# Kernel optimization log

Measured on AMD Instinct MI355X. Metric: run time of the kernel, lower is better.

Reference implementation:

```python
import jax, jax.numpy as jnp
import numpy as np

B, D, L, H = 256, 512, 64, 300


def setup_inputs() -> dict:
    key = jax.random.key(0)
    ks = jax.random.split(key, 16)
    s = 0.05  # weight init scale to keep activations sane through ReLU chains
    return {
        "x": jax.random.normal(ks[0], (B, D), jnp.float32),
        "eps": jax.random.normal(ks[1], (B, L), jnp.float32),
        "W": jax.random.normal(ks[2], (D, L), jnp.float32) * s,
        "enc1_w": jax.random.normal(ks[3], (H, D), jnp.float32) * s,
        "enc1_b": jax.random.normal(ks[4], (H,), jnp.float32) * s,
        "enc2_w": jax.random.normal(ks[5], (H, H), jnp.float32) * s,
        "enc2_b": jax.random.normal(ks[6], (H,), jnp.float32) * s,
        "zm_w": jax.random.normal(ks[7], (L, H), jnp.float32) * s,
        "zm_b": jax.random.normal(ks[8], (L,), jnp.float32) * s,
        "zv_w": jax.random.normal(ks[9], (L, H), jnp.float32) * s,
        "zv_b": jax.random.normal(ks[10], (L,), jnp.float32) * s,
        "gen1_w": jax.random.normal(ks[11], (H, L), jnp.float32) * s,
        "gen2_w": jax.random.normal(ks[12], (H, H), jnp.float32) * s,
        "gen2_b": jax.random.normal(ks[13], (H,), jnp.float32) * s,
        "head_w": jax.random.normal(ks[14], (D, H), jnp.float32) * s,
        "head_b": jax.random.normal(ks[15], (D,), jnp.float32) * s,
    }


def reference(x, eps, W, enc1_w, enc1_b, enc2_w, enc2_b, zm_w, zm_b,
              zv_w, zv_b, gen1_w, gen2_w, gen2_b, head_w, head_b):
    # encode: q_z = ReLU(Linear) -> ReLU(Linear)
    h = jax.nn.relu(x @ enc1_w.T + enc1_b)
    h = jax.nn.relu(h @ enc2_w.T + enc2_b)
    z_mean = h @ zm_w.T + zm_b          # [B, L]
    z_log_var = h @ zv_w.T + zv_b       # [B, L]
    # reparameterize (eps passed in for determinism)
    z = z_mean + eps * jnp.exp(0.5 * z_log_var)
    # decode: per-column masked z through shared generator + per-column head,
    # vectorized over the column axis D (mask = W rows)
    masked = z[:, None, :] * W[None, :, :]                       # [B, D, L]
    g1 = jax.nn.relu(jnp.einsum('bdl,hl->bdh', masked, gen1_w))  # [B, D, H]
    g2 = jax.nn.relu(jnp.einsum('bdh,gh->bdg', g1, gen2_w) + gen2_b)
    x_mean = jnp.einsum('bdh,dh->bd', g2, head_w) + head_b       # [B, D]
    return (x_mean, z, z_mean, z_log_var)
```

## Files before the change

### kernel.cpp

```cpp
#include <hip/hip_runtime.h>

typedef unsigned short u16;
typedef unsigned int u32;

typedef __bf16 bf16x8 __attribute__((ext_vector_type(8)));
typedef float f32x4 __attribute__((ext_vector_type(4)));

union V16 { uint4 u; bf16x8 v; u16 s[8]; };
union F4  { float4 v; float f[4]; };

__device__ __forceinline__ float bf2f(u16 a) {
  union { u32 u; float f; } c; c.u = ((u32)a) << 16; return c.f;
}
__device__ __forceinline__ u16 f2bf(float f) {
  union { float f; u32 u; } c; c.f = f;
  u32 u = c.u;
  u += 0x7fffu + ((u >> 16) & 1u);
  return (u16)(u >> 16);
}

#define Z_OFF   131072
#define ZM_OFF  147456
#define ZLV_OFF 163840

#define B1_OFF 0
#define B2_OFF 2560
#define E1_OFF 15360
#define E2_OFF 35840
#define ZMP_OFF 48640
#define ZVP_OFF 51200
#define PACK_TOTAL 53760

__device__ __forceinline__ void pack_one(const float* __restrict__ src,
                                         int t, int s, int lane,
                                         int Nsrc, int Ksrc, int rowlen,
                                         uint4* __restrict__ dst) {
  const int n = t * 16 + (lane & 15);
  const int k0 = s * 32 + ((lane >> 4) << 3);
  V16 v;
#pragma unroll
  for (int j = 0; j < 8; ++j) {
    const int k = k0 + j;
    v.s[j] = (n < Nsrc && k < Ksrc) ? f2bf(src[n * rowlen + k]) : (u16)0;
  }
  *dst = v.u;
}

__global__ __launch_bounds__(256) void pack_kernel(
    const float* __restrict__ g1w, const float* __restrict__ g2w,
    const float* __restrict__ e1w, const float* __restrict__ e2w,
    const float* __restrict__ zmw, const float* __restrict__ zvw,
    uint4* __restrict__ ws4) {
  const int idx = blockIdx.x * 256 + threadIdx.x;
  if (idx >= PACK_TOTAL) return;
  const int lane = idx & 63;
  if (idx < B2_OFF) {
    const int f = (idx - B1_OFF) >> 6;
    pack_one(g1w, f >> 1, f & 1, lane, 300, 64, 64, ws4 + idx);
  } else if (idx < E1_OFF) {
    const int f = (idx - B2_OFF) >> 6;
    pack_one(g2w, f / 10, f % 10, lane, 300, 300, 300, ws4 + idx);
  } else if (idx < E2_OFF) {
    const int f = (idx - E1_OFF) >> 6;
    pack_one(e1w, f >> 4, f & 15, lane, 300, 512, 512, ws4 + idx);
  } else if (idx < ZMP_OFF) {
    const int f = (idx - E2_OFF) >> 6;
    pack_one(e2w, f / 10, f % 10, lane, 300, 300, 300, ws4 + idx);
  } else if (idx < ZVP_OFF) {
    const int f = (idx - ZMP_OFF) >> 6;
    pack_one(zmw, f / 10, f % 10, lane, 64, 300, 300, ws4 + idx);
  } else {
    const int f = (idx - ZVP_OFF) >> 6;
    pack_one(zvw, f / 10, f % 10, lane, 64, 300, 300, ws4 + idx);
  }
}

__global__ __launch_bounds__(640, 3) void enc_kernel(
    const float* __restrict__ x, const float* __restrict__ eps,
    const uint4* __restrict__ e1p, const float* __restrict__ e1b,
    const uint4* __restrict__ e2p, const float* __restrict__ e2b,
    const uint4* __restrict__ zmp, const float* __restrict__ zmb,
    const uint4* __restrict__ zvp, const float* __restrict__ zvb,
    float* __restrict__ out) {
  __shared__ u16 h1s[16 * 328];
  __shared__ u16 h2s[16 * 328];
  __shared__ float zms[1024], zlvs[1024];
  const int bi0 = blockIdx.x * 16;
  const int tid = threadIdx.x;
  const int w = tid >> 6, lane = tid & 63, q = lane >> 4, c = lane & 15;

  bf16x8 af[16];
#pragma unroll
  for (int s = 0; s < 16; ++s) {
    const float* px = x + (bi0 + c) * 512 + s * 32 + q * 8;
    F4 a, b; a.v = *(const float4*)px; b.v = *(const float4*)(px + 4);
    V16 m;
#pragma unroll
    for (int j = 0; j < 4; ++j) { m.s[j] = f2bf(a.f[j]); m.s[4 + j] = f2bf(b.f[j]); }
    af[s] = m.v;
  }
  f32x4 acc0 = {0.f, 0.f, 0.f, 0.f}, acc1 = {0.f, 0.f, 0.f, 0.f};
  for (int s = 0; s < 16; ++s) {
    V16 b0, b1;
    b0.u = e1p[((2 * w + 0) * 16 + s) * 64 + lane];
    b1.u = e1p[((2 * w + 1) * 16 + s) * 64 + lane];
    acc0 = __builtin_amdgcn_mfma_f32_16x16x32_bf16(af[s], b0.v, acc0, 0, 0, 0);
    acc1 = __builtin_amdgcn_mfma_f32_16x16x32_bf16(af[s], b1.v, acc1, 0, 0, 0);
  }
#pragma unroll
  for (int tt = 0; tt < 2; ++tt) {
    const f32x4 acc = tt ? acc1 : acc0;
    const int col = (2 * w + tt) * 16 + c;
    const float bias = (col < 300) ? e1b[col] : 0.f;
#pragma unroll
    for (int i = 0; i < 4; ++i)
      h1s[(4 * q + i) * 328 + col] = (col < 300) ? f2bf(fmaxf(acc[i] + bias, 0.f)) : (u16)0;
  }
  __syncthreads();
  acc0 = {0.f, 0.f, 0.f, 0.f}; acc1 = {0.f, 0.f, 0.f, 0.f};
  for (int s = 0; s < 10; ++s) {
    V16 a; a.u = *(const uint4*)&h1s[c * 328 + s * 32 + q * 8];
    V16 b0, b1;
    b0.u = e2p[((2 * w + 0) * 10 + s) * 64 + lane];
    b1.u = e2p[((2 * w + 1) * 10 + s) * 64 + lane];
    acc0 = __builtin_amdgcn_mfma_f32_16x16x32_bf16(a.v, b0.v, acc0, 0, 0, 0);
    acc1 = __builtin_amdgcn_mfma_f32_16x16x32_bf16(a.v, b1.v, acc1, 0, 0, 0);
  }
#pragma unroll
  for (int tt = 0; tt < 2; ++tt) {
    const f32x4 acc = tt ? acc1 : acc0;
    const int col = (2 * w + tt) * 16 + c;
    const float bias = (col < 300) ? e2b[col] : 0.f;
#pragma unroll
    for (int i = 0; i < 4; ++i)
      h2s[(4 * q + i) * 328 + col] = (col < 300) ? f2bf(fmaxf(acc[i] + bias, 0.f)) : (u16)0;
  }
  __syncthreads();
  if (w < 8) {
    const bool is_m = (w < 4);
    const int t = w & 3;
    const uint4* hp = is_m ? zmp : zvp;
    f32x4 a4 = {0.f, 0.f, 0.f, 0.f};
    for (int s = 0; s < 10; ++s) {
      V16 a; a.u = *(const uint4*)&h2s[c * 328 + s * 32 + q * 8];
      V16 b; b.u = hp[(t * 10 + s) * 64 + lane];
      a4 = __builtin_amdgcn_mfma_f32_16x16x32_bf16(a.v, b.v, a4, 0, 0, 0);
    }
    const int col = t * 16 + c;
    const float bias = is_m ? zmb[col] : zvb[col];
    float* dst = is_m ? zms : zlvs;
#pragma unroll
    for (int i = 0; i < 4; ++i) dst[(4 * q + i) * 64 + col] = a4[i] + bias;
  }
  __syncthreads();
  for (int idx = tid; idx < 1024; idx += 640) {
    const int row = idx >> 6, col = idx & 63;
    const int gi = (bi0 + row) * 64 + col;
    const float zm = zms[idx], zlv = zlvs[idx];
    const float zz = zm + eps[gi] * expf(0.5f * zlv);
    out[Z_OFF + gi] = zz;
    out[ZM_OFF + gi] = zm;
    out[ZLV_OFF + gi] = zlv;
  }
}

__global__ __launch_bounds__(640, 3) void dec_kernel(
    const float* __restrict__ z,
    const float* __restrict__ W,
    const uint4* __restrict__ b1p,
    const uint4* __restrict__ b2p,
    const float* __restrict__ g2b,
    const float* __restrict__ hw,
    const float* __restrict__ hb,
    float* __restrict__ xout)
{
  __shared__ u16 g1s[128 * 328];
  __shared__ float xred[5][128];

  const int wg = blockIdx.x;
  const int r0 = wg << 7;
  const int bi = r0 >> 9;
  const int d0 = r0 & 511;
  const int tid = threadIdx.x;
  const int w = tid >> 6;
  const int lane = tid & 63;
  const int q = lane >> 4;
  const int c = lane & 15;
  const int u = w >> 1;
  const int v = w & 1;

  const float* zrow = z + bi * 64;

  bf16x8 bz[4][2];
#pragma unroll
  for (int kf = 0; kf < 2; ++kf) {
    F4 z0, z1;
    z0.v = *(const float4*)(zrow + kf * 32 + q * 8);
    z1.v = *(const float4*)(zrow + kf * 32 + q * 8 + 4);
#pragma unroll
    for (int tt = 0; tt < 4; ++tt) {
      V16 r; r.u = b1p[((4 * u + tt) * 2 + kf) * 64 + lane];
      V16 m;
#pragma unroll
      for (int j = 0; j < 4; ++j) {
        m.s[j]     = f2bf(bf2f(r.s[j])     * z0.f[j]);
        m.s[4 + j] = f2bf(bf2f(r.s[4 + j]) * z1.f[j]);
      }
      bz[tt][kf] = m.v;
    }
  }
  for (int rt = 0; rt < 4; ++rt) {
    const int rowA = v * 64 + rt * 16 + c;
    const float* p = W + (d0 + rowA) * 64 + q * 8;
    bf16x8 af0, af1;
    {
      F4 a, b; V16 m;
      a.v = *(const float4*)p; b.v = *(const float4*)(p + 4);
#pragma unroll
      for (int j = 0; j < 4; ++j) { m.s[j] = f2bf(a.f[j]); m.s[4 + j] = f2bf(b.f[j]); }
      af0 = m.v;
      a.v = *(const float4*)(p + 32); b.v = *(const float4*)(p + 36);
#pragma unroll
      for (int j = 0; j < 4; ++j) { m.s[j] = f2bf(a.f[j]); m.s[4 + j] = f2bf(b.f[j]); }
      af1 = m.v;
    }
    f32x4 acc[4];
#pragma unroll
    for (int tt = 0; tt < 4; ++tt) acc[tt] = {0.f, 0.f, 0.f, 0.f};
#pragma unroll
    for (int tt = 0; tt < 4; ++tt) {
      acc[tt] = __builtin_amdgcn_mfma_f32_16x16x32_bf16(af0, bz[tt][0], acc[tt], 0, 0, 0);
      acc[tt] = __builtin_amdgcn_mfma_f32_16x16x32_bf16(af1, bz[tt][1], acc[tt], 0, 0, 0);
    }
    const int rwb = v * 64 + rt * 16 + 4 * q;
#pragma unroll
    for (int tt = 0; tt < 4; ++tt) {
      const int colb = (4 * u + tt) * 16 + c;
#pragma unroll
      for (int i = 0; i < 4; ++i)
        g1s[(rwb + i) * 328 + colb] = f2bf(fmaxf(acc[tt][i], 0.f));
    }
  }
  __syncthreads();

  f32x4 a3[4][4];
#pragma unroll
  for (int tt = 0; tt < 4; ++tt)
#pragma unroll
    for (int rt = 0; rt < 4; ++rt) a3[tt][rt] = {0.f, 0.f, 0.f, 0.f};
  for (int s = 0; s < 10; ++s) {
    V16 b[4];
#pragma unroll
    for (int tt = 0; tt < 4; ++tt) b[tt].u = b2p[((4 * u + tt) * 10 + s) * 64 + lane];
#pragma unroll
    for (int rt = 0; rt < 4; ++rt) {
      V16 a; a.u = *(const uint4*)&g1s[(v * 64 + rt * 16 + c) * 328 + s * 32 + q * 8];
#pragma unroll
      for (int tt = 0; tt < 4; ++tt)
        a3[tt][rt] = __builtin_amdgcn_mfma_f32_16x16x32_bf16(a.v, b[tt].v, a3[tt][rt], 0, 0, 0);
    }
  }
  float xacc[4][4];
#pragma unroll
  for (int rt = 0; rt < 4; ++rt)
#pragma unroll
    for (int i = 0; i < 4; ++i) xacc[rt][i] = 0.f;
#pragma unroll
  for (int tt = 0; tt < 4; ++tt) {
    const int col = (4 * u + tt) * 16 + c;
    const bool inb = (col < 300);
    const float bias = inb ? g2b[col] : 0.f;
#pragma unroll
    for (int rt = 0; rt < 4; ++rt)
#pragma unroll
      for (int i = 0; i < 4; ++i) {
        const float g2v = fmaxf(a3[tt][rt][i] + bias, 0.f);
        const float h = inb ? hw[(d0 + v * 64 + rt * 16 + 4 * q + i) * 300 + col] : 0.f;
        xacc[rt][i] += g2v * h;
      }
  }
#pragma unroll
  for (int rt = 0; rt < 4; ++rt)
#pragma unroll
    for (int i = 0; i < 4; ++i) {
      float t = xacc[rt][i];
      t += __shfl_xor(t, 1);
      t += __shfl_xor(t, 2);
      t += __shfl_xor(t, 4);
      t += __shfl_xor(t, 8);
      xacc[rt][i] = t;
    }
  if (c < 4) {
#pragma unroll
    for (int rt = 0; rt < 4; ++rt) {
      float t = xacc[rt][0];
      t = (c == 1) ? xacc[rt][1] : t;
      t = (c == 2) ? xacc[rt][2] : t;
      t = (c == 3) ? xacc[rt][3] : t;
      xred[u][v * 64 + rt * 16 + 4 * q + c] = t;
    }
  }
  __syncthreads();
  if (tid < 128) {
    float t = hb[d0 + tid];
#pragma unroll
    for (int uu = 0; uu < 5; ++uu) t += xred[uu][tid];
    xout[r0 + tid] = t;
  }
}

extern "C" void kernel_launch(void* const* d_in, const int* in_sizes, int n_in,
                              void* d_out, int out_size, void* d_ws, size_t ws_size,
                              hipStream_t stream) {
  const float* x   = (const float*)d_in[0];
  const float* eps = (const float*)d_in[1];
  const float* W   = (const float*)d_in[2];
  const float* e1w = (const float*)d_in[3];
  const float* e1b = (const float*)d_in[4];
  const float* e2w = (const float*)d_in[5];
  const float* e2b = (const float*)d_in[6];
  const float* zmw = (const float*)d_in[7];
  const float* zmb = (const float*)d_in[8];
  const float* zvw = (const float*)d_in[9];
  const float* zvb = (const float*)d_in[10];
  const float* g1w = (const float*)d_in[11];
  const float* g2w = (const float*)d_in[12];
  const float* g2b = (const float*)d_in[13];
  const float* hw  = (const float*)d_in[14];
  const float* hb  = (const float*)d_in[15];
  float* out = (float*)d_out;
  uint4* ws4 = (uint4*)d_ws;

  pack_kernel<<<(PACK_TOTAL + 255) / 256, 256, 0, stream>>>(g1w, g2w, e1w, e2w, zmw, zvw, ws4);
  enc_kernel<<<16, 640, 0, stream>>>(x, eps,
                                     ws4 + E1_OFF, e1b, ws4 + E2_OFF, e2b,
                                     ws4 + ZMP_OFF, zmb, ws4 + ZVP_OFF, zvb, out);
  dec_kernel<<<1024, 640, 0, stream>>>(out + Z_OFF, W,
                                       ws4 + B1_OFF, ws4 + B2_OFF,
                                       g2b, hw, hb, out);
}
```

Measured before the change: 194.3 us.

## Split encoder into per-tile kernels, pre-convert W/x to bf16, halve decoder blocks

Replaces the 16-block fused encoder with three small grid-wide kernels (enc1, enc2, heads) that use 64-thread blocks, so the encoder's serial work is spread across many more CUs. The pack kernel now also converts W and x to bf16 once, so the decoder loads ready bf16 fragments instead of converting fp32 per block. The decoder uses 64-row tiles with 320 threads and 2048 blocks to cut LDS per block and raise occupancy. Software bf16 rounding is swapped for native __bf16 casts. In exchange it adds two kernel launches and global round trips for h1/h2, and each decoder block now covers fewer rows.

```diff
diff --git a/kernel.cpp b/kernel.cpp
--- a/kernel.cpp
+++ b/kernel.cpp
@@ -6,17 +6,11 @@
 typedef __bf16 bf16x8 __attribute__((ext_vector_type(8)));
 typedef float f32x4 __attribute__((ext_vector_type(4)));
 
-union V16 { uint4 u; bf16x8 v; u16 s[8]; };
+union V16 { uint4 u; bf16x8 v; u16 s[8]; __bf16 h[8]; };
 union F4  { float4 v; float f[4]; };
 
 __device__ __forceinline__ float bf2f(u16 a) {
   union { u32 u; float f; } c; c.u = ((u32)a) << 16; return c.f;
-}
-__device__ __forceinline__ u16 f2bf(float f) {
-  union { float f; u32 u; } c; c.f = f;
-  u32 u = c.u;
-  u += 0x7fffu + ((u >> 16) & 1u);
-  return (u16)(u >> 16);
 }
 
 #define Z_OFF   131072
@@ -29,7 +23,12 @@
 #define E2_OFF 35840
 #define ZMP_OFF 48640
 #define ZVP_OFF 51200
-#define PACK_TOTAL 53760
+#define FRAG_TOTAL 53760
+#define WB4  53760
+#define XB4  57856
+#define H1_4 74240
+#define H2_4 84480
+#define PACK_THREADS (FRAG_TOTAL + 4096 + 16384)
 
 __device__ __forceinline__ void pack_one(const float* __restrict__ src,
                                          int t, int s, int lane,
@@ -41,8 +40,16 @@
 #pragma unroll
   for (int j = 0; j < 8; ++j) {
     const int k = k0 + j;
-    v.s[j] = (n < Nsrc && k < Ksrc) ? f2bf(src[n * rowlen + k]) : (u16)0;
-  }
+    v.h[j] = (n < Nsrc && k < Ksrc) ? (__bf16)src[n * rowlen + k] : (__bf16)0.f;
+  }
+  *dst = v.u;
+}
+
+__device__ __forceinline__ void cvt8(const float* __restrict__ src, uint4* __restrict__ dst) {
+  F4 a, b; a.v = *(const float4*)src; b.v = *(const float4*)(src + 4);
+  V16 v;
+#pragma unroll
+  for (int j = 0; j < 4; ++j) { v.h[j] = (__bf16)a.f[j]; v.h[4 + j] = (__bf16)b.f[j]; }
   *dst = v.u;
 }
 
@@ -50,9 +57,10 @@
     const float* __restrict__ g1w, const float* __restrict__ g2w,
     const float* __restrict__ e1w, const float* __restrict__ e2w,
     const float* __restrict__ zmw, const float* __restrict__ zvw,
+    const float* __restrict__ W,   const float* __restrict__ x,
     uint4* __restrict__ ws4) {
   const int idx = blockIdx.x * 256 + threadIdx.x;
-  if (idx >= PACK_TOTAL) return;
+  if (idx >= PACK_THREADS) return;
   const int lane = idx & 63;
   if (idx < B2_OFF) {
     const int f = (idx - B1_OFF) >> 6;
@@ -69,125 +77,118 @@
   } else if (idx < ZVP_OFF) {
     const int f = (idx - ZMP_OFF) >> 6;
     pack_one(zmw, f / 10, f % 10, lane, 64, 300, 300, ws4 + idx);
-  } else {
+  } else if (idx < FRAG_TOTAL) {
     const int f = (idx - ZVP_OFF) >> 6;
     pack_one(zvw, f / 10, f % 10, lane, 64, 300, 300, ws4 + idx);
-  }
-}
-
-__global__ __launch_bounds__(640, 3) void enc_kernel(
-    const float* __restrict__ x, const float* __restrict__ eps,
-    const uint4* __restrict__ e1p, const float* __restrict__ e1b,
-    const uint4* __restrict__ e2p, const float* __restrict__ e2b,
+  } else if (idx < FRAG_TOTAL + 4096) {
+    const int i = idx - FRAG_TOTAL;
+    cvt8(W + i * 8, ws4 + WB4 + i);
+  } else {
+    const int i = idx - FRAG_TOTAL - 4096;
+    cvt8(x + i * 8, ws4 + XB4 + i);
+  }
+}
+
+__global__ __launch_bounds__(64) void enc1_kernel(
+    const uint4* __restrict__ xb, const uint4* __restrict__ e1p,
+    const float* __restrict__ e1b, u16* __restrict__ h1) {
+  const int wg = blockIdx.x;
+  const int rt = wg / 20, nt = wg % 20;
+  const int lane = threadIdx.x, q = lane >> 4, c = lane & 15;
+  f32x4 acc = {0.f, 0.f, 0.f, 0.f};
+  const int arow = rt * 16 + c;
+  for (int s = 0; s < 16; ++s) {
+    V16 a, b;
+    a.u = xb[arow * 64 + s * 4 + q];
+    b.u = e1p[(nt * 16 + s) * 64 + lane];
+    acc = __builtin_amdgcn_mfma_f32_16x16x32_bf16(a.v, b.v, acc, 0, 0, 0);
+  }
+  const int col = nt * 16 + c;
+  const float bias = (col < 300) ? e1b[col] : 0.f;
+#pragma unroll
+  for (int i = 0; i < 4; ++i) {
+    const int row = rt * 16 + 4 * q + i;
+    V16 t; t.h[0] = (col < 300) ? (__bf16)fmaxf(acc[i] + bias, 0.f) : (__bf16)0.f;
+    h1[row * 320 + col] = t.s[0];
+  }
+}
+
+__global__ __launch_bounds__(64) void enc2_kernel(
+    const uint4* __restrict__ h1, const uint4* __restrict__ e2p,
+    const float* __restrict__ e2b, u16* __restrict__ h2) {
+  const int wg = blockIdx.x;
+  const int rt = wg / 20, nt = wg % 20;
+  const int lane = threadIdx.x, q = lane >> 4, c = lane & 15;
+  f32x4 acc = {0.f, 0.f, 0.f, 0.f};
+  const int arow = rt * 16 + c;
+  for (int s = 0; s < 10; ++s) {
+    V16 a, b;
+    a.u = h1[arow * 40 + s * 4 + q];
+    b.u = e2p[(nt * 10 + s) * 64 + lane];
+    acc = __builtin_amdgcn_mfma_f32_16x16x32_bf16(a.v, b.v, acc, 0, 0, 0);
+  }
+  const int col = nt * 16 + c;
+  const float bias = (col < 300) ? e2b[col] : 0.f;
+#pragma unroll
+  for (int i = 0; i < 4; ++i) {
+    const int row = rt * 16 + 4 * q + i;
+    V16 t; t.h[0] = (col < 300) ? (__bf16)fmaxf(acc[i] + bias, 0.f) : (__bf16)0.f;
+    h2[row * 320 + col] = t.s[0];
+  }
+}
+
+__global__ __launch_bounds__(64) void ench_kernel(
+    const uint4* __restrict__ h2, const float* __restrict__ eps,
     const uint4* __restrict__ zmp, const float* __restrict__ zmb,
     const uint4* __restrict__ zvp, const float* __restrict__ zvb,
     float* __restrict__ out) {
-  __shared__ u16 h1s[16 * 328];
-  __shared__ u16 h2s[16 * 328];
-  __shared__ float zms[1024], zlvs[1024];
-  const int bi0 = blockIdx.x * 16;
-  const int tid = threadIdx.x;
-  const int w = tid >> 6, lane = tid & 63, q = lane >> 4, c = lane & 15;
-
-  bf16x8 af[16];
-#pragma unroll
-  for (int s = 0; s < 16; ++s) {
-    const float* px = x + (bi0 + c) * 512 + s * 32 + q * 8;
-    F4 a, b; a.v = *(const float4*)px; b.v = *(const float4*)(px + 4);
-    V16 m;
-#pragma unroll
-    for (int j = 0; j < 4; ++j) { m.s[j] = f2bf(a.f[j]); m.s[4 + j] = f2bf(b.f[j]); }
-    af[s] = m.v;
-  }
-  f32x4 acc0 = {0.f, 0.f, 0.f, 0.f}, acc1 = {0.f, 0.f, 0.f, 0.f};
-  for (int s = 0; s < 16; ++s) {
-    V16 b0, b1;
-    b0.u = e1p[((2 * w + 0) * 16 + s) * 64 + lane];
-    b1.u = e1p[((2 * w + 1) * 16 + s) * 64 + lane];
-    acc0 = __builtin_amdgcn_mfma_f32_16x16x32_bf16(af[s], b0.v, acc0, 0, 0, 0);
-    acc1 = __builtin_amdgcn_mfma_f32_16x16x32_bf16(af[s], b1.v, acc1, 0, 0, 0);
-  }
-#pragma unroll
-  for (int tt = 0; tt < 2; ++tt) {
-    const f32x4 acc = tt ? acc1 : acc0;
-    const int col = (2 * w + tt) * 16 + c;
-    const float bias = (col < 300) ? e1b[col] : 0.f;
-#pragma unroll
-    for (int i = 0; i < 4; ++i)
-      h1s[(4 * q + i) * 328 + col] = (col < 300) ? f2bf(fmaxf(acc[i] + bias, 0.f)) : (u16)0;
-  }
-  __syncthreads();
-  acc0 = {0.f, 0.f, 0.f, 0.f}; acc1 = {0.f, 0.f, 0.f, 0.f};
+  const int wg = blockIdx.x;
+  const int rt = wg >> 2, t = wg & 3;
+  const int lane = threadIdx.x, q = lane >> 4, c = lane & 15;
+  f32x4 am = {0.f, 0.f, 0.f, 0.f}, av = {0.f, 0.f, 0.f, 0.f};
+  const int arow = rt * 16 + c;
   for (int s = 0; s < 10; ++s) {
-    V16 a; a.u = *(const uint4*)&h1s[c * 328 + s * 32 + q * 8];
-    V16 b0, b1;
-    b0.u = e2p[((2 * w + 0) * 10 + s) * 64 + lane];
-    b1.u = e2p[((2 * w + 1) * 10 + s) * 64 + lane];
-    acc0 = __builtin_amdgcn_mfma_f32_16x16x32_bf16(a.v, b0.v, acc0, 0, 0, 0);
-    acc1 = __builtin_amdgcn_mfma_f32_16x16x32_bf16(a.v, b1.v, acc1, 0, 0, 0);
-  }
-#pragma unroll
-  for (int tt = 0; tt < 2; ++tt) {
-    const f32x4 acc = tt ? acc1 : acc0;
-    const int col = (2 * w + tt) * 16 + c;
-    const float bias = (col < 300) ? e2b[col] : 0.f;
-#pragma unroll
-    for (int i = 0; i < 4; ++i)
-      h2s[(4 * q + i) * 328 + col] = (col < 300) ? f2bf(fmaxf(acc[i] + bias, 0.f)) : (u16)0;
-  }
-  __syncthreads();
-  if (w < 8) {
-    const bool is_m = (w < 4);
-    const int t = w & 3;
-    const uint4* hp = is_m ? zmp : zvp;
-    f32x4 a4 = {0.f, 0.f, 0.f, 0.f};
-    for (int s = 0; s < 10; ++s) {
-      V16 a; a.u = *(const uint4*)&h2s[c * 328 + s * 32 + q * 8];
-      V16 b; b.u = hp[(t * 10 + s) * 64 + lane];
-      a4 = __builtin_amdgcn_mfma_f32_16x16x32_bf16(a.v, b.v, a4, 0, 0, 0);
-    }
-    const int col = t * 16 + c;
-    const float bias = is_m ? zmb[col] : zvb[col];
-    float* dst = is_m ? zms : zlvs;
-#pragma unroll
-    for (int i = 0; i < 4; ++i) dst[(4 * q + i) * 64 + col] = a4[i] + bias;
-  }
-  __syncthreads();
-  for (int idx = tid; idx < 1024; idx += 640) {
-    const int row = idx >> 6, col = idx & 63;
-    const int gi = (bi0 + row) * 64 + col;
-    const float zm = zms[idx], zlv = zlvs[idx];
-    const float zz = zm + eps[gi] * expf(0.5f * zlv);
-    out[Z_OFF + gi] = zz;
+    V16 a, bm, bv;
+    a.u = h2[arow * 40 + s * 4 + q];
+    bm.u = zmp[(t * 10 + s) * 64 + lane];
+    bv.u = zvp[(t * 10 + s) * 64 + lane];
+    am = __builtin_amdgcn_mfma_f32_16x16x32_bf16(a.v, bm.v, am, 0, 0, 0);
+    av = __builtin_amdgcn_mfma_f32_16x16x32_bf16(a.v, bv.v, av, 0, 0, 0);
+  }
+  const int col = t * 16 + c;
+  const float bm = zmb[col], bv = zvb[col];
+#pragma unroll
+  for (int i = 0; i < 4; ++i) {
+    const int gi = (rt * 16 + 4 * q + i) * 64 + col;
+    const float zm = am[i] + bm;
+    const float zlv = av[i] + bv;
     out[ZM_OFF + gi] = zm;
     out[ZLV_OFF + gi] = zlv;
-  }
-}
-
-__global__ __launch_bounds__(640, 3) void dec_kernel(
+    out[Z_OFF + gi] = zm + eps[gi] * expf(0.5f * zlv);
+  }
+}
+
+__global__ __launch_bounds__(320, 3) void dec_kernel(
     const float* __restrict__ z,
-    const float* __restrict__ W,
+    const uint4* __restrict__ Wb,
     const uint4* __restrict__ b1p,
     const uint4* __restrict__ b2p,
     const float* __restrict__ g2b,
     const float* __restrict__ hw,
     const float* __restrict__ hb,
-    float* __restrict__ xout)
-{
-  __shared__ u16 g1s[128 * 328];
-  __shared__ float xred[5][128];
+    float* __restrict__ xout) {
+  __shared__ u16 g1s[64 * 328];
+  __shared__ float xred[5][64];
 
   const int wg = blockIdx.x;
-  const int r0 = wg << 7;
+  const int r0 = wg << 6;
   const int bi = r0 >> 9;
   const int d0 = r0 & 511;
   const int tid = threadIdx.x;
-  const int w = tid >> 6;
+  const int u = tid >> 6;
   const int lane = tid & 63;
   const int q = lane >> 4;
   const int c = lane & 15;
-  const int u = w >> 1;
-  const int v = w & 1;
 
   const float* zrow = z + bi * 64;
 
@@ -203,42 +204,34 @@
       V16 m;
 #pragma unroll
       for (int j = 0; j < 4; ++j) {
-        m.s[j]     = f2bf(bf2f(r.s[j])     * z0.f[j]);
-        m.s[4 + j] = f2bf(bf2f(r.s[4 + j]) * z1.f[j]);
+        m.h[j]     = (__bf16)(bf2f(r.s[j])     * z0.f[j]);
+        m.h[4 + j] = (__bf16)(bf2f(r.s[4 + j]) * z1.f[j]);
       }
       bz[tt][kf] = m.v;
     }
   }
   for (int rt = 0; rt < 4; ++rt) {
-    const int rowA = v * 64 + rt * 16 + c;
-    const float* p = W + (d0 + rowA) * 64 + q * 8;
-    bf16x8 af0, af1;
-    {
-      F4 a, b; V16 m;
-      a.v = *(const float4*)p; b.v = *(const float4*)(p + 4);
-#pragma unroll
-      for (int j = 0; j < 4; ++j) { m.s[j] = f2bf(a.f[j]); m.s[4 + j] = f2bf(b.f[j]); }
-      af0 = m.v;
-      a.v = *(const float4*)(p + 32); b.v = *(const float4*)(p + 36);
-#pragma unroll
-      for (int j = 0; j < 4; ++j) { m.s[j] = f2bf(a.f[j]); m.s[4 + j] = f2bf(b.f[j]); }
-      af1 = m.v;
-    }
+    const int rowA = rt * 16 + c;
+    V16 af0, af1;
+    af0.u = Wb[(d0 + rowA) * 8 + q];
+    af1.u = Wb[(d0 + rowA) * 8 + 4 + q];
     f32x4 acc[4];
 #pragma unroll
     for (int tt = 0; tt < 4; ++tt) acc[tt] = {0.f, 0.f, 0.f, 0.f};
 #pragma unroll
     for (int tt = 0; tt < 4; ++tt) {
-      acc[tt] = __builtin_amdgcn_mfma_f32_16x16x32_bf16(af0, bz[tt][0], acc[tt], 0, 0, 0);
-      acc[tt] = __builtin_amdgcn_mfma_f32_16x16x32_bf16(af1, bz[tt][1], acc[tt], 0, 0, 0);
-    }
-    const int rwb = v * 64 + rt * 16 + 4 * q;
+      acc[tt] = __builtin_amdgcn_mfma_f32_16x16x32_bf16(af0.v, bz[tt][0], acc[tt], 0, 0, 0);
+      acc[tt] = __builtin_amdgcn_mfma_f32_16x16x32_bf16(af1.v, bz[tt][1], acc[tt], 0, 0, 0);
+    }
+    const int rwb = rt * 16 + 4 * q;
 #pragma unroll
     for (int tt = 0; tt < 4; ++tt) {
       const int colb = (4 * u + tt) * 16 + c;
 #pragma unroll
-      for (int i = 0; i < 4; ++i)
-        g1s[(rwb + i) * 328 + colb] = f2bf(fmaxf(acc[tt][i], 0.f));
+      for (int i = 0; i < 4; ++i) {
+        V16 t; t.h[0] = (__bf16)fmaxf(acc[tt][i], 0.f);
+        g1s[(rwb + i) * 328 + colb] = t.s[0];
+      }
     }
   }
   __syncthreads();
@@ -254,7 +247,7 @@
     for (int tt = 0; tt < 4; ++tt) b[tt].u = b2p[((4 * u + tt) * 10 + s) * 64 + lane];
 #pragma unroll
     for (int rt = 0; rt < 4; ++rt) {
-      V16 a; a.u = *(const uint4*)&g1s[(v * 64 + rt * 16 + c) * 328 + s * 32 + q * 8];
+      V16 a; a.u = *(const uint4*)&g1s[(rt * 16 + c) * 328 + s * 32 + q * 8];
 #pragma unroll
       for (int tt = 0; tt < 4; ++tt)
         a3[tt][rt] = __builtin_amdgcn_mfma_f32_16x16x32_bf16(a.v, b[tt].v, a3[tt][rt], 0, 0, 0);
@@ -275,7 +268,7 @@
 #pragma unroll
       for (int i = 0; i < 4; ++i) {
         const float g2v = fmaxf(a3[tt][rt][i] + bias, 0.f);
-        const float h = inb ? hw[(d0 + v * 64 + rt * 16 + 4 * q + i) * 300 + col] : 0.f;
+        const float h = inb ? hw[(d0 + rt * 16 + 4 * q + i) * 300 + col] : 0.f;
         xacc[rt][i] += g2v * h;
       }
   }
@@ -297,11 +290,11 @@
       t = (c == 1) ? xacc[rt][1] : t;
       t = (c == 2) ? xacc[rt][2] : t;
       t = (c == 3) ? xacc[rt][3] : t;
-      xred[u][v * 64 + rt * 16 + 4 * q + c] = t;
+      xred[u][rt * 16 + 4 * q + c] = t;
     }
   }
   __syncthreads();
-  if (tid < 128) {
+  if (tid < 64) {
     float t = hb[d0 + tid];
 #pragma unroll
     for (int uu = 0; uu < 5; ++uu) t += xred[uu][tid];
@@ -331,11 +324,13 @@
   float* out = (float*)d_out;
   uint4* ws4 = (uint4*)d_ws;
 
-  pack_kernel<<<(PACK_TOTAL + 255) / 256, 256, 0, stream>>>(g1w, g2w, e1w, e2w, zmw, zvw, ws4);
-  enc_kernel<<<16, 640, 0, stream>>>(x, eps,
-                                     ws4 + E1_OFF, e1b, ws4 + E2_OFF, e2b,
+  pack_kernel<<<(PACK_THREADS + 255) / 256, 256, 0, stream>>>(
+      g1w, g2w, e1w, e2w, zmw, zvw, W, x, ws4);
+  enc1_kernel<<<320, 64, 0, stream>>>(ws4 + XB4, ws4 + E1_OFF, e1b, (u16*)(ws4 + H1_4));
+  enc2_kernel<<<320, 64, 0, stream>>>(ws4 + H1_4, ws4 + E2_OFF, e2b, (u16*)(ws4 + H2_4));
+  ench_kernel<<<64, 64, 0, stream>>>(ws4 + H2_4, eps,
                                      ws4 + ZMP_OFF, zmb, ws4 + ZVP_OFF, zvb, out);
-  dec_kernel<<<1024, 640, 0, stream>>>(out + Z_OFF, W,
+  dec_kernel<<<2048, 320, 0, stream>>>(out + Z_OFF, ws4 + WB4,
                                        ws4 + B1_OFF, ws4 + B2_OFF,
                                        g2b, hw, hb, out);
 }
```

Result: faster. 184.0 us (-5.3%).
